# Kernel optimization log

Measured on AMD Instinct MI355X. Metric: run time of the kernel, lower is better.

The kernel has to match this reference:

```python
import jax, jax.numpy as jnp
import numpy as np

D_MODEL = 1024
N_HEADS = 16
HDIM = D_MODEL // N_HEADS
IMP_EPS = 1e-6


def setup_inputs() -> dict:
    key = jax.random.key(0)
    ks = jax.random.split(key, 7)
    B, T_q, T_kv, N_s = 2, 2048, 256, 16
    scale = 1.0 / np.sqrt(D_MODEL)
    return {
        "query": jax.random.normal(ks[0], (B, T_q, D_MODEL), dtype=jnp.float32),
        "key_value": jax.random.normal(ks[1], (B, T_kv, N_s, D_MODEL), dtype=jnp.float32),
        "imp_weights": jax.random.uniform(ks[2], (B, N_s), dtype=jnp.float32),
        "W_q": jax.random.normal(ks[3], (D_MODEL, D_MODEL), dtype=jnp.float32) * scale,
        "W_k": jax.random.normal(ks[4], (D_MODEL, D_MODEL), dtype=jnp.float32) * scale,
        "W_v": jax.random.normal(ks[5], (D_MODEL, D_MODEL), dtype=jnp.float32) * scale,
        "W_o": jax.random.normal(ks[6], (D_MODEL, D_MODEL), dtype=jnp.float32) * scale,
    }


def _split_heads(x):
    # [B, T, D] -> [B, h, T, d]
    B, T, _ = x.shape
    return x.reshape(B, T, N_HEADS, HDIM).transpose(0, 2, 1, 3)


def reference(query, key_value, imp_weights, W_q, W_k, W_v, W_o):
    # CAU_MultiheadCrossAttention.forward with 4D key_value (sensor axis).
    B, T_q, D = query.shape
    _, T_kv, N_s, _ = key_value.shape
    kv = key_value.reshape(B, T_kv * N_s, D)  # flatten sensor axis into source length S

    qh = _split_heads(query @ W_q.T)   # [B,h,T_q,d]  (nn.Linear: x @ W.T)
    kh = _split_heads(kv @ W_k.T)      # [B,h,S,d]
    vh = _split_heads(kv @ W_v.T)      # [B,h,S,d]

    # importance: [B,N_s] -> tiled over T_kv -> [B, S], log-clamped additive mask
    imp_full = jnp.broadcast_to(imp_weights[:, None, :], (B, T_kv, N_s)).reshape(B, T_kv * N_s)
    log_imp = jnp.log(jnp.clip(imp_full, IMP_EPS, None)).astype(qh.dtype)  # [B,S]

    scores = jnp.einsum("bhqd,bhkd->bhqk", qh, kh) / np.sqrt(HDIM).astype(np.float32)
    scores = scores + log_imp[:, None, None, :]
    attn = jax.nn.softmax(scores, axis=-1)
    y = jnp.einsum("bhqk,bhkd->bhqd", attn, vh)  # [B,h,T_q,d]

    y = y.transpose(0, 2, 1, 3).reshape(B, T_q, D)  # merge heads
    return y @ W_o.T
```

## Files before the change

kernel.cpp:

```cpp
#include <hip/hip_runtime.h>
#include <hip/hip_bf16.h>

typedef __bf16    bf16x8_t __attribute__((ext_vector_type(8)));
typedef __bf16    bf16x4_t __attribute__((ext_vector_type(4)));
typedef float     f32x4_t  __attribute__((ext_vector_type(4)));
typedef _Float16  f16x8_t  __attribute__((ext_vector_type(8)));

static __device__ __forceinline__ f32x4_t mfma16(bf16x8_t a, bf16x8_t b, f32x4_t c) {
    return __builtin_amdgcn_mfma_f32_16x16x32_bf16(a, b, c, 0, 0, 0);
}

static __device__ __forceinline__ float redsum16(float v) {
#pragma unroll
    for (int off = 1; off < 16; off <<= 1) v += __shfl_xor(v, off);
    return v;
}

static __device__ __forceinline__ void async16(const __bf16* g, __bf16* l) {
    __builtin_amdgcn_global_load_lds(
        (const __attribute__((address_space(1))) unsigned int*)g,
        (__attribute__((address_space(3))) unsigned int*)l, 16, 0, 0);
}

__global__ __launch_bounds__(256) void f2b_multi(const float* __restrict__ q,
                                                 const float* __restrict__ kv,
                                                 const float* __restrict__ wq,
                                                 const float* __restrict__ wk,
                                                 const float* __restrict__ wv,
                                                 const float* __restrict__ wo,
                                                 __bf16* __restrict__ qb,
                                                 __bf16* __restrict__ kvb,
                                                 __bf16* __restrict__ wqb,
                                                 __bf16* __restrict__ wkvb,
                                                 __bf16* __restrict__ wob,
                                                 float qscale) {
    int i = blockIdx.x * 256 + threadIdx.x;
    const float* src; __bf16* dst; int base; float scale = 1.0f;
    if (i < 1048576)      { src = q;  dst = qb;   base = 0; }
    else if (i < 3145728) { src = kv; dst = kvb;  base = 1048576; }
    else if (i < 3407872) { src = wq; dst = wqb;  base = 3145728; scale = qscale; }
    else if (i < 3670016) { src = wk; dst = wkvb; base = 3407872; }
    else if (i < 3932160) { src = wv; dst = wkvb + 1048576; base = 3670016; }
    else                  { src = wo; dst = wob;  base = 3932160; }
    int j = i - base;
    float4 v = reinterpret_cast<const float4*>(src)[j];
    bf16x4_t o;
    o[0] = (__bf16)(v.x * scale); o[1] = (__bf16)(v.y * scale);
    o[2] = (__bf16)(v.z * scale); o[3] = (__bf16)(v.w * scale);
    reinterpret_cast<bf16x4_t*>(dst)[j] = o;
}

__global__ __launch_bounds__(256) void proj_kernel(const __bf16* __restrict__ qb,
                                                   const __bf16* __restrict__ wqb,
                                                   const __bf16* __restrict__ kvb,
                                                   const __bf16* __restrict__ wkvb,
                                                   __bf16* __restrict__ Qp,
                                                   __bf16* __restrict__ Khd,
                                                   __bf16* __restrict__ Vhd,
                                                   const float* __restrict__ imp) {
    __shared__ __bf16 As[128 * 32];
    __shared__ __bf16 Bs[128 * 32];
    __shared__ __bf16 Es[2][4096];

    const int gid = blockIdx.x;
    const __bf16 *A, *B;
    long m0, n0;
    int mode;
    if (gid < 256) {
        m0 = (long)(gid >> 3) * 128; n0 = (long)(gid & 7) * 128;
        A = qb; B = wqb; mode = 0;
    } else {
        int g2 = gid - 256;
        m0 = (long)(g2 >> 4) * 128; n0 = (long)(g2 & 15) * 128;
        A = kvb; B = wkvb; mode = (n0 < 1024) ? 1 : 2;
    }

    const int t    = threadIdx.x;
    const int w    = t >> 6;
    const int lane = t & 63;
    const int quad = lane >> 4;
    const int mn   = lane & 15;
    const int wm   = (w & 1) * 64;
    const int wn   = (w >> 1) * 64;

    const int  srow = t >> 2;
    const int  scol = (t & 3) * 8;
    const __bf16* gA = A + (m0 + srow) * 1024 + scol;
    const __bf16* gB = B + (n0 + srow) * 1024 + scol;

    f32x4_t acc[4][4];
#pragma unroll
    for (int i = 0; i < 4; i++)
#pragma unroll
        for (int j = 0; j < 4; j++) acc[i][j] = (f32x4_t){0.f, 0.f, 0.f, 0.f};

    for (int k0 = 0; k0 < 1024; k0 += 32) {
        __syncthreads();
        async16(gA + k0,              &As[t * 8]);
        async16(gA + 64 * 1024 + k0,  &As[2048 + t * 8]);
        async16(gB + k0,              &Bs[t * 8]);
        async16(gB + 64 * 1024 + k0,  &Bs[2048 + t * 8]);
        __syncthreads();

        bf16x8_t af[4], bf[4];
#pragma unroll
        for (int i = 0; i < 4; i++)
            af[i] = *(const bf16x8_t*)&As[(wm + i * 16 + mn) * 32 + quad * 8];
#pragma unroll
        for (int j = 0; j < 4; j++)
            bf[j] = *(const bf16x8_t*)&Bs[(wn + j * 16 + mn) * 32 + quad * 8];
#pragma unroll
        for (int i = 0; i < 4; i++)
#pragma unroll
            for (int j = 0; j < 4; j++) acc[i][j] = mfma16(af[i], bf[j], acc[i][j]);
    }

    __syncthreads();
    __bf16* stg = (w == 0) ? As : (w == 1) ? Bs : Es[w - 2];

    if (mode != 2) {
#pragma unroll
        for (int i = 0; i < 4; i++)
#pragma unroll
            for (int j = 0; j < 4; j++)
#pragma unroll
                for (int r = 0; r < 4; r++) {
                    int sl = i * 16 + quad * 4 + r;
                    int d  = j * 16 + mn;
                    stg[sl * 64 + (((d >> 3) ^ (sl & 7)) * 8) + (d & 7)] =
                        (__bf16)acc[i][j][r];
                }
    } else {
        const int b_ = (int)((m0 + wm) >> 12);
#pragma unroll
        for (int r = 0; r < 4; r++) {
            float scl = fmaxf(imp[b_ * 16 + quad * 4 + r], 1e-6f);
#pragma unroll
            for (int j = 0; j < 4; j++) {
                bf16x4_t pk;
#pragma unroll
                for (int i = 0; i < 4; i++) pk[i] = (__bf16)(acc[i][j][r] * scl);
                int d  = j * 16 + mn;
                int p0 = (quad * 4 + r) * 4;
                *(bf16x4_t*)&stg[d * 64 + (((p0 >> 3) ^ (d & 7)) * 8) + (p0 & 7)] = pk;
            }
        }
    }

    if (mode == 0) {
        __bf16* Cg = Qp + (m0 + wm) * 1024 + (n0 + wn);
#pragma unroll
        for (int it = 0; it < 8; it++) {
            int rowL = it * 8 + (lane >> 3);
            int cb   = lane & 7;
            bf16x8_t vv = *(const bf16x8_t*)&stg[rowL * 64 + ((cb ^ (rowL & 7)) * 8)];
            *(bf16x8_t*)&Cg[(long)rowL * 1024 + cb * 8] = vv;
        }
    } else {
        const int b_    = (int)((m0 + wm) >> 12);
        const int sbase = (int)((m0 + wm) & 4095);
        __bf16* dst;
        if (mode == 1) {
            int h_ = (int)((n0 + wn) >> 6);
            dst = Khd + (long)(b_ * 16 + h_) * 262144 + (long)sbase * 64;
        } else {
            int h_ = (int)((n0 + wn) >> 6) - 16;
            dst = Vhd + (long)(b_ * 16 + h_) * 262144 + (long)(sbase >> 6) * 4096;
        }
#pragma unroll
        for (int it = 0; it < 8; it++) {
            int rowL = it * 8 + (lane >> 3);
            int cb   = lane & 7;
            bf16x8_t vv = *(const bf16x8_t*)&stg[rowL * 64 + ((cb ^ (rowL & 7)) * 8)];
            *(bf16x8_t*)&dst[rowL * 64 + cb * 8] = vv;
        }
    }
}

__global__ __launch_bounds__(256) void attn_kernel(const __bf16* __restrict__ Qp,
                                                   const __bf16* __restrict__ Kh,
                                                   const __bf16* __restrict__ Vh,
                                                   const float* __restrict__ imp,
                                                   _Float16* __restrict__ Op,
                                                   float* __restrict__ Lp) {
    const int gid = blockIdx.x;
    const int qt  = (gid >> 3) & 15;
    const int sp  = (gid >> 7) & 1;
    const int bh  = ((gid >> 8) << 3) | (gid & 7);
    const int b   = bh >> 4;
    const int h   = bh & 15;
    const int t    = threadIdx.x;
    const int w    = t >> 6;
    const int lane = t & 63;
    const int quad = lane >> 4;
    const int mn   = lane & 15;

    __shared__ __bf16 Ks[2][4096];
    __shared__ __bf16 Vs[2][4096];
    __shared__ __bf16 Ps[4][32][72];

    const long qrow0 = (long)b * 2048 + qt * 128 + w * 32;
    const __bf16* Kb = Kh + (long)bh * 262144;
    const __bf16* Vb = Vh + (long)bh * 262144;

    const int r8 = lane >> 3;
    const int cs = (lane & 7) ^ r8;
    const int srcoff0 = (0 * 4 + w) * 512 + r8 * 64 + cs * 8;
    const int srcoff1 = (1 * 4 + w) * 512 + r8 * 64 + cs * 8;

    bf16x8_t aq[2][2];
#pragma unroll
    for (int rt = 0; rt < 2; rt++)
#pragma unroll
        for (int x = 0; x < 2; x++)
            aq[rt][x] = *(const bf16x8_t*)&Qp[(qrow0 + rt * 16 + mn) * 1024 + h * 64 + x * 32 + quad * 8];

    const float impc = fmaxf(imp[b * 16 + mn], 1e-6f);

    float lpart[2][4];
    f32x4_t o[2][4];
#pragma unroll
    for (int rt = 0; rt < 2; rt++)
#pragma unroll
        for (int r = 0; r < 4; r++) lpart[rt][r] = 0.f;
#pragma unroll
    for (int rt = 0; rt < 2; rt++)
#pragma unroll
        for (int dt = 0; dt < 4; dt++) o[rt][dt] = (f32x4_t){0.f, 0.f, 0.f, 0.f};

    {
        const long kbase = (long)(sp * 32) * 4096;
        async16(Kb + kbase + srcoff0, &Ks[0][(0 * 4 + w) * 512]);
        async16(Kb + kbase + srcoff1, &Ks[0][(1 * 4 + w) * 512]);
        async16(Vb + kbase + srcoff0, &Vs[0][(0 * 4 + w) * 512]);
        async16(Vb + kbase + srcoff1, &Vs[0][(1 * 4 + w) * 512]);
    }

    for (int ii = 0; ii < 32; ii++) {
        const int bi = ii & 1;
        __syncthreads();

        if (ii + 1 < 32) {
            const long kbase = (long)(sp * 32 + ii + 1) * 4096;
            async16(Kb + kbase + srcoff0, &Ks[bi ^ 1][(0 * 4 + w) * 512]);
            async16(Kb + kbase + srcoff1, &Ks[bi ^ 1][(1 * 4 + w) * 512]);
            async16(Vb + kbase + srcoff0, &Vs[bi ^ 1][(0 * 4 + w) * 512]);
            async16(Vb + kbase + srcoff1, &Vs[bi ^ 1][(1 * 4 + w) * 512]);
        }

        f32x4_t sc[2][4];
        {
            bf16x8_t bk0[4], bk1[4];
#pragma unroll
            for (int ct = 0; ct < 4; ct++) {
                int s  = ct * 16 + mn;
                int c0 = (quad ^ (s & 7)) * 8;
                bk0[ct] = *(const bf16x8_t*)&Ks[bi][s * 64 + c0];
                bk1[ct] = *(const bf16x8_t*)&Ks[bi][s * 64 + (c0 ^ 32)];
            }
#pragma unroll
            for (int rt = 0; rt < 2; rt++) {
#pragma unroll
                for (int ct = 0; ct < 4; ct++) sc[rt][ct] = (f32x4_t){0.f, 0.f, 0.f, 0.f};
#pragma unroll
                for (int ct = 0; ct < 4; ct++) {
                    sc[rt][ct] = mfma16(aq[rt][0], bk0[ct], sc[rt][ct]);
                    sc[rt][ct] = mfma16(aq[rt][1], bk1[ct], sc[rt][ct]);
                }
            }
        }

#pragma unroll
        for (int rt = 0; rt < 2; rt++)
#pragma unroll
            for (int r = 0; r < 4; r++) {
                float p0 = __builtin_amdgcn_exp2f(sc[rt][0][r]);
                float p1 = __builtin_amdgcn_exp2f(sc[rt][1][r]);
                float p2 = __builtin_amdgcn_exp2f(sc[rt][2][r]);
                float p3 = __builtin_amdgcn_exp2f(sc[rt][3][r]);
                lpart[rt][r] += (p0 + p1) + (p2 + p3);
                bf16x4_t pk;
                pk[0] = (__bf16)p0; pk[1] = (__bf16)p1;
                pk[2] = (__bf16)p2; pk[3] = (__bf16)p3;
                *(bf16x4_t*)&Ps[w][rt * 16 + quad * 4 + r][mn * 4] = pk;
            }

        {
            bf16x8_t bv0[4], bv1[4];
#pragma unroll
            for (int dt = 0; dt < 4; dt++) {
                int d  = dt * 16 + mn;
                int c0 = (quad ^ (d & 7)) * 8;
                bv0[dt] = *(const bf16x8_t*)&Vs[bi][d * 64 + c0];
                bv1[dt] = *(const bf16x8_t*)&Vs[bi][d * 64 + (c0 ^ 32)];
            }
#pragma unroll
            for (int rt = 0; rt < 2; rt++) {
                bf16x8_t ap0 = *(const bf16x8_t*)&Ps[w][rt * 16 + mn][quad * 8];
                bf16x8_t ap1 = *(const bf16x8_t*)&Ps[w][rt * 16 + mn][32 + quad * 8];
#pragma unroll
                for (int dt = 0; dt < 4; dt++) {
                    o[rt][dt] = mfma16(ap0, bv0[dt], o[rt][dt]);
                    o[rt][dt] = mfma16(ap1, bv1[dt], o[rt][dt]);
                }
            }
        }
    }

#pragma unroll
    for (int rt = 0; rt < 2; rt++)
#pragma unroll
        for (int r = 0; r < 4; r++) {
            float l = redsum16(lpart[rt][r] * impc);
            long row = qrow0 + rt * 16 + quad * 4 + r;
            if (mn == 0) Lp[((long)sp * 4096 + row) * 16 + h] = l;
#pragma unroll
            for (int dt = 0; dt < 4; dt++)
                Op[((long)sp * 4096 + row) * 1024 + h * 64 + dt * 16 + mn] =
                    (_Float16)o[rt][dt][r];
        }
}

__global__ __launch_bounds__(256) void combine_kernel(const _Float16* __restrict__ Op,
                                                      const float* __restrict__ Lp,
                                                      __bf16* __restrict__ Y) {
    int tid = blockIdx.x * 256 + threadIdx.x;
    int row = tid >> 7;
    int cg  = tid & 127;
    int h   = cg >> 3;
    f16x8_t o0 = *(const f16x8_t*)&Op[(long)row * 1024 + cg * 8];
    f16x8_t o1 = *(const f16x8_t*)&Op[(long)(4096 + row) * 1024 + cg * 8];
    float inv = 1.0f / (Lp[row * 16 + h] + Lp[(4096 + row) * 16 + h]);
    bf16x8_t y;
#pragma unroll
    for (int j = 0; j < 8; j++) y[j] = (__bf16)(((float)o0[j] + (float)o1[j]) * inv);
    *(bf16x8_t*)&Y[(long)row * 1024 + cg * 8] = y;
}

__global__ __launch_bounds__(256) void gemm_out_kernel(const __bf16* __restrict__ A,
                                                       const __bf16* __restrict__ B,
                                                       float* __restrict__ C) {
    __shared__ __bf16 As[128 * 32];
    __shared__ __bf16 Bs[128 * 32];

    const int t    = threadIdx.x;
    const int w    = t >> 6;
    const int lane = t & 63;
    const int quad = lane >> 4;
    const int mn   = lane & 15;
    const int wm   = (w & 1) * 64;
    const int wn   = (w >> 1) * 64;
    const long m0  = (long)blockIdx.y * 128;
    const long n0  = (long)blockIdx.x * 128;

    const int  srow = t >> 2;
    const int  scol = (t & 3) * 8;
    const __bf16* gA = A + (m0 + srow) * 1024 + scol;
    const __bf16* gB = B + (n0 + srow) * 1024 + scol;

    f32x4_t acc[4][4];
#pragma unroll
    for (int i = 0; i < 4; i++)
#pragma unroll
        for (int j = 0; j < 4; j++) acc[i][j] = (f32x4_t){0.f, 0.f, 0.f, 0.f};

    for (int k0 = 0; k0 < 1024; k0 += 32) {
        __syncthreads();
        async16(gA + k0,             &As[t * 8]);
        async16(gA + 64 * 1024 + k0, &As[2048 + t * 8]);
        async16(gB + k0,             &Bs[t * 8]);
        async16(gB + 64 * 1024 + k0, &Bs[2048 + t * 8]);
        __syncthreads();

        bf16x8_t af[4], bf[4];
#pragma unroll
        for (int i = 0; i < 4; i++)
            af[i] = *(const bf16x8_t*)&As[(wm + i * 16 + mn) * 32 + quad * 8];
#pragma unroll
        for (int j = 0; j < 4; j++)
            bf[j] = *(const bf16x8_t*)&Bs[(wn + j * 16 + mn) * 32 + quad * 8];
#pragma unroll
        for (int i = 0; i < 4; i++)
#pragma unroll
            for (int j = 0; j < 4; j++) acc[i][j] = mfma16(af[i], bf[j], acc[i][j]);
    }

#pragma unroll
    for (int i = 0; i < 4; i++)
#pragma unroll
        for (int j = 0; j < 4; j++)
#pragma unroll
            for (int r = 0; r < 4; r++) {
                long row = m0 + wm + i * 16 + quad * 4 + r;
                long col = n0 + wn + j * 16 + mn;
                C[row * 1024 + col] = acc[i][j][r];
            }
}

extern "C" void kernel_launch(void* const* d_in, const int* in_sizes, int n_in,
                              void* d_out, int out_size, void* d_ws, size_t ws_size,
                              hipStream_t stream) {
    const float* q_f  = (const float*)d_in[0];
    const float* kv_f = (const float*)d_in[1];
    const float* imp  = (const float*)d_in[2];
    const float* wq_f = (const float*)d_in[3];
    const float* wk_f = (const float*)d_in[4];
    const float* wv_f = (const float*)d_in[5];
    const float* wo_f = (const float*)d_in[6];

    char* ws = (char*)d_ws;
    const size_t MB = 1ull << 20;
    __bf16*   qb    = (__bf16*)(ws + 0);
    __bf16*   kvb   = (__bf16*)(ws + 8 * MB);
    __bf16*   wqb   = (__bf16*)(ws + 24 * MB);
    __bf16*   wkvb  = (__bf16*)(ws + 26 * MB);
    _Float16* Opart = (_Float16*)(ws + 0);
    float*    Lpart = (float*)(ws + 16 * MB);
    __bf16*   Yb    = (__bf16*)(ws + 17 * MB);
    __bf16*   wob   = (__bf16*)(ws + 30 * MB);
    __bf16*   Qp    = (__bf16*)(ws + 32 * MB);
    __bf16*   Khd   = (__bf16*)(ws + 40 * MB);
    __bf16*   Vhd   = (__bf16*)(ws + 56 * MB);

    const float QSCALE = 0.125f * 1.4426950408889634f;

    f2b_multi<<<16384, 256, 0, stream>>>(q_f, kv_f, wq_f, wk_f, wv_f, wo_f,
                                         qb, kvb, wqb, wkvb, wob, QSCALE);

    proj_kernel<<<1280, 256, 0, stream>>>(qb, wqb, kvb, wkvb, Qp, Khd, Vhd, imp);

    attn_kernel<<<1024, 256, 0, stream>>>(Qp, Khd, Vhd, imp, Opart, Lpart);
    combine_kernel<<<2048, 256, 0, stream>>>(Opart, Lpart, Yb);

    gemm_out_kernel<<<dim3(8, 32), 256, 0, stream>>>(Yb, wob, (float*)d_out);
}
```

Baseline: 304.3 us.

## Single-buffer attention LDS for occupancy and split-K the output GEMM

The attention kernel drops double-buffered K/V staging in shared memory and asks for four blocks per CU through launch bounds. Each KV tile is now loaded synchronously between two barriers, so less global-load latency is overlapped. The output projection GEMM is split along K into two halves that write fp32 partials into scratch space. A new elementwise kernel then sums the two partials into the output, doubling the GEMM block count for better CU fill at the cost of extra partial-sum traffic and one more launch.

```diff
diff --git a/kernel.cpp b/kernel.cpp
--- a/kernel.cpp
+++ b/kernel.cpp
@@ -177,12 +177,12 @@
     }
 }
 
-__global__ __launch_bounds__(256) void attn_kernel(const __bf16* __restrict__ Qp,
-                                                   const __bf16* __restrict__ Kh,
-                                                   const __bf16* __restrict__ Vh,
-                                                   const float* __restrict__ imp,
-                                                   _Float16* __restrict__ Op,
-                                                   float* __restrict__ Lp) {
+__global__ __launch_bounds__(256, 4) void attn_kernel(const __bf16* __restrict__ Qp,
+                                                      const __bf16* __restrict__ Kh,
+                                                      const __bf16* __restrict__ Vh,
+                                                      const float* __restrict__ imp,
+                                                      _Float16* __restrict__ Op,
+                                                      float* __restrict__ Lp) {
     const int gid = blockIdx.x;
     const int qt  = (gid >> 3) & 15;
     const int sp  = (gid >> 7) & 1;
@@ -195,8 +195,8 @@
     const int quad = lane >> 4;
     const int mn   = lane & 15;
 
-    __shared__ __bf16 Ks[2][4096];
-    __shared__ __bf16 Vs[2][4096];
+    __shared__ __bf16 Ks[64 * 64];
+    __shared__ __bf16 Vs[64 * 64];
     __shared__ __bf16 Ps[4][32][72];
 
     const long qrow0 = (long)b * 2048 + qt * 128 + w * 32;
@@ -207,6 +207,10 @@
     const int cs = (lane & 7) ^ r8;
     const int srcoff0 = (0 * 4 + w) * 512 + r8 * 64 + cs * 8;
     const int srcoff1 = (1 * 4 + w) * 512 + r8 * 64 + cs * 8;
+    __bf16* ldsK0 = Ks + (0 * 4 + w) * 512;
+    __bf16* ldsK1 = Ks + (1 * 4 + w) * 512;
+    __bf16* ldsV0 = Vs + (0 * 4 + w) * 512;
+    __bf16* ldsV1 = Vs + (1 * 4 + w) * 512;
 
     bf16x8_t aq[2][2];
 #pragma unroll
@@ -228,25 +232,14 @@
 #pragma unroll
         for (int dt = 0; dt < 4; dt++) o[rt][dt] = (f32x4_t){0.f, 0.f, 0.f, 0.f};
 
-    {
-        const long kbase = (long)(sp * 32) * 4096;
-        async16(Kb + kbase + srcoff0, &Ks[0][(0 * 4 + w) * 512]);
-        async16(Kb + kbase + srcoff1, &Ks[0][(1 * 4 + w) * 512]);
-        async16(Vb + kbase + srcoff0, &Vs[0][(0 * 4 + w) * 512]);
-        async16(Vb + kbase + srcoff1, &Vs[0][(1 * 4 + w) * 512]);
-    }
-
-    for (int ii = 0; ii < 32; ii++) {
-        const int bi = ii & 1;
-        __syncthreads();
-
-        if (ii + 1 < 32) {
-            const long kbase = (long)(sp * 32 + ii + 1) * 4096;
-            async16(Kb + kbase + srcoff0, &Ks[bi ^ 1][(0 * 4 + w) * 512]);
-            async16(Kb + kbase + srcoff1, &Ks[bi ^ 1][(1 * 4 + w) * 512]);
-            async16(Vb + kbase + srcoff0, &Vs[bi ^ 1][(0 * 4 + w) * 512]);
-            async16(Vb + kbase + srcoff1, &Vs[bi ^ 1][(1 * 4 + w) * 512]);
-        }
+    for (int st = sp * 32; st < sp * 32 + 32; st++) {
+        const long kbase = (long)st * 4096;
+        __syncthreads();
+        async16(Kb + kbase + srcoff0, ldsK0);
+        async16(Kb + kbase + srcoff1, ldsK1);
+        async16(Vb + kbase + srcoff0, ldsV0);
+        async16(Vb + kbase + srcoff1, ldsV1);
+        __syncthreads();
 
         f32x4_t sc[2][4];
         {
@@ -255,8 +248,8 @@
             for (int ct = 0; ct < 4; ct++) {
                 int s  = ct * 16 + mn;
                 int c0 = (quad ^ (s & 7)) * 8;
-                bk0[ct] = *(const bf16x8_t*)&Ks[bi][s * 64 + c0];
-                bk1[ct] = *(const bf16x8_t*)&Ks[bi][s * 64 + (c0 ^ 32)];
+                bk0[ct] = *(const bf16x8_t*)&Ks[s * 64 + c0];
+                bk1[ct] = *(const bf16x8_t*)&Ks[s * 64 + (c0 ^ 32)];
             }
 #pragma unroll
             for (int rt = 0; rt < 2; rt++) {
@@ -291,8 +284,8 @@
             for (int dt = 0; dt < 4; dt++) {
                 int d  = dt * 16 + mn;
                 int c0 = (quad ^ (d & 7)) * 8;
-                bv0[dt] = *(const bf16x8_t*)&Vs[bi][d * 64 + c0];
-                bv1[dt] = *(const bf16x8_t*)&Vs[bi][d * 64 + (c0 ^ 32)];
+                bv0[dt] = *(const bf16x8_t*)&Vs[d * 64 + c0];
+                bv1[dt] = *(const bf16x8_t*)&Vs[d * 64 + (c0 ^ 32)];
             }
 #pragma unroll
             for (int rt = 0; rt < 2; rt++) {
@@ -339,9 +332,15 @@
 
 __global__ __launch_bounds__(256) void gemm_out_kernel(const __bf16* __restrict__ A,
                                                        const __bf16* __restrict__ B,
-                                                       float* __restrict__ C) {
+                                                       float* __restrict__ P) {
     __shared__ __bf16 As[128 * 32];
     __shared__ __bf16 Bs[128 * 32];
+
+    const int  kh = blockIdx.x >> 3;
+    const long n0 = (long)(blockIdx.x & 7) * 128;
+    const long m0 = (long)blockIdx.y * 128;
+    const int  kb = kh * 512;
+    float* C = P + (long)kh * 4194304;
 
     const int t    = threadIdx.x;
     const int w    = t >> 6;
@@ -350,13 +349,11 @@
     const int mn   = lane & 15;
     const int wm   = (w & 1) * 64;
     const int wn   = (w >> 1) * 64;
-    const long m0  = (long)blockIdx.y * 128;
-    const long n0  = (long)blockIdx.x * 128;
 
     const int  srow = t >> 2;
     const int  scol = (t & 3) * 8;
-    const __bf16* gA = A + (m0 + srow) * 1024 + scol;
-    const __bf16* gB = B + (n0 + srow) * 1024 + scol;
+    const __bf16* gA = A + (m0 + srow) * 1024 + kb + scol;
+    const __bf16* gB = B + (n0 + srow) * 1024 + kb + scol;
 
     f32x4_t acc[4][4];
 #pragma unroll
@@ -364,7 +361,7 @@
 #pragma unroll
         for (int j = 0; j < 4; j++) acc[i][j] = (f32x4_t){0.f, 0.f, 0.f, 0.f};
 
-    for (int k0 = 0; k0 < 1024; k0 += 32) {
+    for (int k0 = 0; k0 < 512; k0 += 32) {
         __syncthreads();
         async16(gA + k0,             &As[t * 8]);
         async16(gA + 64 * 1024 + k0, &As[2048 + t * 8]);
@@ -395,6 +392,16 @@
                 long col = n0 + wn + j * 16 + mn;
                 C[row * 1024 + col] = acc[i][j][r];
             }
+}
+
+__global__ __launch_bounds__(256) void combine2_kernel(const float* __restrict__ P0,
+                                                       const float* __restrict__ P1,
+                                                       float* __restrict__ out) {
+    int i = blockIdx.x * 256 + threadIdx.x;
+    float4 a = reinterpret_cast<const float4*>(P0)[i];
+    float4 b = reinterpret_cast<const float4*>(P1)[i];
+    float4 c; c.x = a.x + b.x; c.y = a.y + b.y; c.z = a.z + b.z; c.w = a.w + b.w;
+    reinterpret_cast<float4*>(out)[i] = c;
 }
 
 extern "C" void kernel_launch(void* const* d_in, const int* in_sizes, int n_in,
@@ -421,6 +428,7 @@
     __bf16*   Qp    = (__bf16*)(ws + 32 * MB);
     __bf16*   Khd   = (__bf16*)(ws + 40 * MB);
     __bf16*   Vhd   = (__bf16*)(ws + 56 * MB);
+    float*    Gp    = (float*)(ws + 40 * MB);
 
     const float QSCALE = 0.125f * 1.4426950408889634f;
 
@@ -432,5 +440,6 @@
     attn_kernel<<<1024, 256, 0, stream>>>(Qp, Khd, Vhd, imp, Opart, Lpart);
     combine_kernel<<<2048, 256, 0, stream>>>(Opart, Lpart, Yb);
 
-    gemm_out_kernel<<<dim3(8, 32), 256, 0, stream>>>(Yb, wob, (float*)d_out);
-}
+    gemm_out_kernel<<<dim3(16, 32), 256, 0, stream>>>(Yb, wob, Gp);
+    combine2_kernel<<<4096, 256, 0, stream>>>(Gp, Gp + 4194304, (float*)d_out);
+}
```

Result: faster. 288.7 us (-5.1%).
